# Kernel tuning notes

Measured on AMD Instinct MI355X. Metric: run time of the kernel, lower is better.

Reference implementation:

```python
import jax, jax.numpy as jnp
import numpy as np

HID = 512
J = 64
NEG = -1e9


def _gru_cell(x, h, Wih, Whh, bih, bhh):
    # PyTorch GRUCell: gates stacked as (r, z, n) along first dim of (3H, in)
    gi = Wih @ x + bih          # (3H,)
    gh = Whh @ h + bhh          # (3H,)
    r = jax.nn.sigmoid(gi[:HID] + gh[:HID])
    z = jax.nn.sigmoid(gi[HID:2 * HID] + gh[HID:2 * HID])
    n = jnp.tanh(gi[2 * HID:] + r * gh[2 * HID:])
    return (1.0 - z) * n + z * h


def setup_inputs() -> dict:
    key = jax.random.key(0)
    ks = jax.random.split(key, 8)
    T = 4096
    state_dim = 2 * J  # input is state[t][1:]
    d = {
        "state": jax.random.normal(ks[0], (T, state_dim + 1), dtype=jnp.float32),
        "h_prev": jnp.zeros((2, HID), dtype=jnp.float32),
        "mask": jax.random.randint(ks[1], (J, J), 0, 2, dtype=jnp.int32),
        "Wih0": jax.random.normal(ks[2], (3 * HID, state_dim), dtype=jnp.float32) * 0.05,
        "Whh0": jax.random.normal(ks[3], (3 * HID, HID), dtype=jnp.float32) * 0.04,
        "bih0": jnp.zeros((3 * HID,), dtype=jnp.float32),
        "bhh0": jnp.zeros((3 * HID,), dtype=jnp.float32),
        "Wih1": jax.random.normal(ks[4], (3 * HID, HID), dtype=jnp.float32) * 0.04,
        "Whh1": jax.random.normal(ks[5], (3 * HID, HID), dtype=jnp.float32) * 0.04,
        "bih1": jnp.zeros((3 * HID,), dtype=jnp.float32),
        "bhh1": jnp.zeros((3 * HID,), dtype=jnp.float32),
        "Wfc": jax.random.normal(ks[6], (J * J, HID), dtype=jnp.float32) * 0.06,
        "bfc": jnp.zeros((J * J,), dtype=jnp.float32),
    }
    return d


def reference(state, h_prev, mask, Wih0, Whh0, bih0, bhh0,
              Wih1, Whh1, bih1, bhh1, Wfc, bfc):
    xs = state[:, 1:]  # drop leading element, matches state[t][1:]

    def step(hs, x_t):
        h0 = _gru_cell(x_t, hs[0], Wih0, Whh0, bih0, bhh0)
        h1 = _gru_cell(h0, hs[1], Wih1, Whh1, bih1, bhh1)
        new = jnp.stack([h0, h1])
        return new, h1

    h_next, h_list = jax.lax.scan(step, h_prev, xs)  # h_list: (T, HID)
    logits = jax.nn.relu(h_list @ Wfc.T + bfc)       # (T, J*J)
    logits = logits.reshape(-1, J, J)
    logits = jnp.where(mask == 0, jnp.float32(NEG), logits)
    return logits, h_next
```

## Files before the change

### kernel.cpp

```cpp
#include <hip/hip_runtime.h>
#include <stdint.h>

#define TSTEPS   4096
#define NEG_VAL  -1000000000.0f
#define NWG_SCAN 96
#define G0WG     32
#define RINGN    32

#define GI0_OFF   0
#define H1_OFF    (TSTEPS*1536*4)
#define RING0_OFF (H1_OFF + TSTEPS*512*4)
#define RING1_OFF (RING0_OFF + RINGN*512*8)
#define ARR_OFF   (RING1_OFF + RINGN*512*8)
#define WS_NEED   ((size_t)ARR_OFF + RINGN*64)

static __device__ __forceinline__ unsigned long long ld_a64(const unsigned long long* p){
  return __hip_atomic_load(p, __ATOMIC_RELAXED, __HIP_MEMORY_SCOPE_AGENT);
}
static __device__ __forceinline__ void st_a64(unsigned long long* p, unsigned long long v){
  __hip_atomic_store(p, v, __ATOMIC_RELAXED, __HIP_MEMORY_SCOPE_AGENT);
}
static __device__ __forceinline__ float sigmoidf_(float x){
  return 1.0f / (1.0f + __expf(-x));
}
static __device__ __forceinline__ float tanhf_(float x){
  float ax = fabsf(x);
  float e  = __expf(-2.0f*ax);
  float t  = (1.0f - e) / (1.0f + e);
  return copysignf(t, x);
}

static __device__ __forceinline__ void spin_to_lds(const unsigned long long* ring, int slot,
                                                   unsigned want, int lane, float* dst,
                                                   long* budget){
  const unsigned long long* bp = ring + (size_t)slot*512 + lane;
  unsigned long long v[8];
  for(;;){
    #pragma unroll
    for (int j=0;j<8;++j) v[j] = ld_a64(bp + j*64);
    bool ok = true;
    #pragma unroll
    for (int j=0;j<8;++j) ok = ok && ((unsigned)(v[j]>>32) == want);
    if (ok) break;
    if (--(*budget) < 0) break;
  }
  #pragma unroll
  for (int j=0;j<8;++j) dst[j*64+lane] = __uint_as_float((unsigned)v[j]);
}

__global__ __launch_bounds__(384,1) void gru_scan(
    const float* __restrict__ gi0,
    const float* __restrict__ hprev,
    const float* __restrict__ Whh0,
    const float* __restrict__ Wih1,
    const float* __restrict__ Whh1,
    const float* __restrict__ bhh0,
    const float* __restrict__ bih1,
    const float* __restrict__ bhh1,
    float* __restrict__ H1hist,
    unsigned long long* ring0,
    unsigned long long* ring1,
    unsigned* arr,
    float* __restrict__ hnext)
{
  const int wg   = blockIdx.x;
  const int tid  = threadIdx.x;
  const int wave = tid >> 6;
  const int lane = tid & 63;

  __shared__ float hbuf0[512];
  __shared__ float hbuf1[512];
  __shared__ float sc[64];

  long budget = (1L<<22);

  if (wg < G0WG) {
    const int ibase = wg*16;
    float w[8][8];
    #pragma unroll
    for (int k=0;k<8;++k){
      const int rid = wave*8+k;
      const int g = rid>>4, il = rid&15;
      const float* wp = Whh0 + ((size_t)(g*512 + ibase + il))*512;
      #pragma unroll
      for (int j=0;j<8;++j) w[k][j] = wp[j*64 + lane];
    }
    float hreg=0.f, br=0.f, bz=0.f, bn_=0.f;
    const int mi = ibase + tid;
    if (tid < 16){
      hreg = hprev[mi];
      br  = bhh0[mi]; bz = bhh0[512+mi]; bn_ = bhh0[1024+mi];
    }
    for (int t=0; t<TSTEPS; ++t){
      float gr=0.f, gz=0.f, gn=0.f;
      if (tid < 16){
        const float* gp = gi0 + (size_t)t*1536 + mi;
        gr = gp[0]; gz = gp[512]; gn = gp[1024];
      }
      if (wave == 0){
        if (t == 0){
          #pragma unroll
          for (int j=0;j<8;++j) hbuf0[j*64+lane] = hprev[j*64+lane];
        } else {
          spin_to_lds(ring0, (t-1)&(RINGN-1), (unsigned)t, lane, hbuf0, &budget);
        }
      }
      if (tid==0 && t>=16){
        unsigned* ap = arr + (size_t)((t-16)&(RINGN-1))*16;
        const unsigned expect = (unsigned)NWG_SCAN * (unsigned)(((t-16)>>5)+1);
        while (__hip_atomic_load(ap, __ATOMIC_RELAXED, __HIP_MEMORY_SCOPE_AGENT) < expect){
          if (--budget < 0) break;
        }
      }
      __syncthreads();
      float hj[8];
      #pragma unroll
      for (int j=0;j<8;++j) hj[j] = hbuf0[j*64+lane];
      float acc[8];
      #pragma unroll
      for (int k=0;k<8;++k){
        float a = 0.f;
        #pragma unroll
        for (int j=0;j<8;++j) a = fmaf(w[k][j], hj[j], a);
        #pragma unroll
        for (int off=32; off; off>>=1) a += __shfl_xor(a, off, 64);
        acc[k] = a;
      }
      if (lane == 0){
        #pragma unroll
        for (int k=0;k<8;++k) sc[wave*8+k] = acc[k];
      }
      __syncthreads();
      if (tid < 16){
        const float ghr = sc[tid]    + br;
        const float ghz = sc[16+tid] + bz;
        const float ghn = sc[32+tid] + bn_;
        const float r = sigmoidf_(gr + ghr);
        const float z = sigmoidf_(gz + ghz);
        const float n = tanhf_(gn + r*ghn);
        const float h = (1.f - z)*n + z*hreg;
        hreg = h;
        st_a64(ring0 + (size_t)(t&(RINGN-1))*512 + mi,
               ((unsigned long long)(unsigned)(t+1)<<32) |
               (unsigned long long)__float_as_uint(h));
        if (t == TSTEPS-1) hnext[mi] = h;
      }
      __syncthreads();
      if (tid == 0){
        __hip_atomic_fetch_add(arr + (size_t)(t&(RINGN-1))*16, 1u,
                               __ATOMIC_RELEASE, __HIP_MEMORY_SCOPE_AGENT);
      }
    }
  } else {
    const int wgl = wg - G0WG;
    const int ibase = wgl*8;
    const bool isA = (wave < 3);
    float w[8][8];
    #pragma unroll
    for (int k=0;k<8;++k){
      const int rid = (isA ? wave : (wave-3))*8 + k;
      const int g = rid>>3, il = rid&7;
      const float* W = isA ? Wih1 : Whh1;
      const float* wp = W + ((size_t)(g*512 + ibase + il))*512;
      #pragma unroll
      for (int j=0;j<8;++j) w[k][j] = wp[j*64 + lane];
    }
    float hreg=0.f, bir=0.f,biz=0.f,bin_=0.f, bhr=0.f,bhz=0.f,bhn=0.f;
    const int mi = ibase + tid;
    if (tid < 8){
      hreg = hprev[512+mi];
      bir = bih1[mi]; biz = bih1[512+mi]; bin_ = bih1[1024+mi];
      bhr = bhh1[mi]; bhz = bhh1[512+mi]; bhn  = bhh1[1024+mi];
    }
    for (int s=0; s<TSTEPS; ++s){
      if (wave == 0){
        spin_to_lds(ring0, s&(RINGN-1), (unsigned)(s+1), lane, hbuf0, &budget);
      } else if (wave == 3){
        if (s == 0){
          #pragma unroll
          for (int j=0;j<8;++j) hbuf1[j*64+lane] = hprev[512 + j*64+lane];
        } else {
          spin_to_lds(ring1, (s-1)&(RINGN-1), (unsigned)s, lane, hbuf1, &budget);
        }
      }
      if (tid==0 && s>=16){
        unsigned* ap = arr + (size_t)((s-16)&(RINGN-1))*16;
        const unsigned expect = (unsigned)NWG_SCAN * (unsigned)(((s-16)>>5)+1);
        while (__hip_atomic_load(ap, __ATOMIC_RELAXED, __HIP_MEMORY_SCOPE_AGENT) < expect){
          if (--budget < 0) break;
        }
      }
      __syncthreads();
      const float* hsrc = isA ? hbuf0 : hbuf1;
      float hj[8];
      #pragma unroll
      for (int j=0;j<8;++j) hj[j] = hsrc[j*64+lane];
      float acc[8];
      #pragma unroll
      for (int k=0;k<8;++k){
        float a = 0.f;
        #pragma unroll
        for (int j=0;j<8;++j) a = fmaf(w[k][j], hj[j], a);
        #pragma unroll
        for (int off=32; off; off>>=1) a += __shfl_xor(a, off, 64);
        acc[k] = a;
      }
      if (lane == 0){
        const int base = isA ? (wave*8) : (24 + (wave-3)*8);
        #pragma unroll
        for (int k=0;k<8;++k) sc[base+k] = acc[k];
      }
      __syncthreads();
      if (tid < 8){
        const float gir = sc[tid]    + bir;
        const float giz = sc[8+tid]  + biz;
        const float gin = sc[16+tid] + bin_;
        const float ghr = sc[24+tid] + bhr;
        const float ghz = sc[32+tid] + bhz;
        const float ghn = sc[40+tid] + bhn;
        const float r = sigmoidf_(gir + ghr);
        const float z = sigmoidf_(giz + ghz);
        const float n = tanhf_(gin + r*ghn);
        const float h = (1.f - z)*n + z*hreg;
        hreg = h;
        st_a64(ring1 + (size_t)(s&(RINGN-1))*512 + mi,
               ((unsigned long long)(unsigned)(s+1)<<32) |
               (unsigned long long)__float_as_uint(h));
        H1hist[(size_t)s*512 + mi] = h;
        if (s == TSTEPS-1) hnext[512+mi] = h;
      }
      __syncthreads();
      if (tid == 0){
        __hip_atomic_fetch_add(arr + (size_t)(s&(RINGN-1))*16, 1u,
                               __ATOMIC_RELEASE, __HIP_MEMORY_SCOPE_AGENT);
      }
    }
  }
}

template<int EPI>
__global__ __launch_bounds__(256) void gemm_nt(
    const float* __restrict__ A, int lda,
    const float* __restrict__ B, int ldb,
    float* __restrict__ C, int ldc,
    const float* __restrict__ bias,
    const int* __restrict__ mask,
    int K)
{
  __shared__ __align__(16) float As[32][68];
  __shared__ __align__(16) float Bs[32][68];
  const int bm = blockIdx.y*64, bn = blockIdx.x*64;
  const int tid = threadIdx.x;
  const int tm = tid>>4, tn = tid&15;
  float acc[4][4] = {};
  const int m0 = tid>>2, kk0 = (tid&3)*8;
  for (int k0=0; k0<K; k0+=32){
    #pragma unroll
    for (int j=0;j<8;++j) As[kk0+j][m0] = A[(size_t)(bm+m0)*lda + k0+kk0+j];
    #pragma unroll
    for (int j=0;j<8;++j) Bs[kk0+j][m0] = B[(size_t)(bn+m0)*ldb + k0+kk0+j];
    __syncthreads();
    #pragma unroll
    for (int kk=0;kk<32;++kk){
      const float4 av = *(const float4*)&As[kk][tm*4];
      const float4 bv = *(const float4*)&Bs[kk][tn*4];
      acc[0][0]=fmaf(av.x,bv.x,acc[0][0]); acc[0][1]=fmaf(av.x,bv.y,acc[0][1]);
      acc[0][2]=fmaf(av.x,bv.z,acc[0][2]); acc[0][3]=fmaf(av.x,bv.w,acc[0][3]);
      acc[1][0]=fmaf(av.y,bv.x,acc[1][0]); acc[1][1]=fmaf(av.y,bv.y,acc[1][1]);
      acc[1][2]=fmaf(av.y,bv.z,acc[1][2]); acc[1][3]=fmaf(av.y,bv.w,acc[1][3]);
      acc[2][0]=fmaf(av.z,bv.x,acc[2][0]); acc[2][1]=fmaf(av.z,bv.y,acc[2][1]);
      acc[2][2]=fmaf(av.z,bv.z,acc[2][2]); acc[2][3]=fmaf(av.z,bv.w,acc[2][3]);
      acc[3][0]=fmaf(av.w,bv.x,acc[3][0]); acc[3][1]=fmaf(av.w,bv.y,acc[3][1]);
      acc[3][2]=fmaf(av.w,bv.z,acc[3][2]); acc[3][3]=fmaf(av.w,bv.w,acc[3][3]);
    }
    __syncthreads();
  }
  #pragma unroll
  for (int i=0;i<4;++i){
    #pragma unroll
    for (int j=0;j<4;++j){
      const int mm = bm + tm*4 + i, cc = bn + tn*4 + j;
      float v = acc[i][j] + bias[cc];
      if (EPI){
        v = fmaxf(v, 0.f);
        if (mask[cc] == 0) v = NEG_VAL;
      }
      C[(size_t)mm*ldc + cc] = v;
    }
  }
}

extern "C" void kernel_launch(void* const* d_in, const int* in_sizes, int n_in,
                              void* d_out, int out_size, void* d_ws, size_t ws_size,
                              hipStream_t stream)
{
  const float* state = (const float*)d_in[0];
  const float* hprev = (const float*)d_in[1];
  const int*   mask  = (const int*)d_in[2];
  const float* Wih0  = (const float*)d_in[3];
  const float* Whh0  = (const float*)d_in[4];
  const float* bih0  = (const float*)d_in[5];
  const float* bhh0  = (const float*)d_in[6];
  const float* Wih1  = (const float*)d_in[7];
  const float* Whh1  = (const float*)d_in[8];
  const float* bih1  = (const float*)d_in[9];
  const float* bhh1  = (const float*)d_in[10];
  const float* Wfc   = (const float*)d_in[11];
  const float* bfc   = (const float*)d_in[12];

  if (ws_size < WS_NEED) return;

  float* out = (float*)d_out;
  char*  ws  = (char*)d_ws;
  float* gi0 = (float*)(ws + GI0_OFF);
  float* H1  = (float*)(ws + H1_OFF);
  unsigned long long* ring0 = (unsigned long long*)(ws + RING0_OFF);
  unsigned long long* ring1 = (unsigned long long*)(ws + RING1_OFF);
  unsigned* arr = (unsigned*)(ws + ARR_OFF);

  (void)hipMemsetAsync(ws + RING0_OFF, 0, (size_t)(WS_NEED - RING0_OFF), stream);

  {
    dim3 grid(1536/64, 4096/64);
    gemm_nt<0><<<grid, 256, 0, stream>>>(state+1, 129, Wih0, 128, gi0, 1536,
                                         bih0, nullptr, 128);
  }

  gru_scan<<<NWG_SCAN, 384, 0, stream>>>(gi0, hprev, Whh0, Wih1, Whh1,
                                         bhh0, bih1, bhh1,
                                         H1, ring0, ring1, arr,
                                         out + (size_t)4096*4096);

  {
    dim3 grid(4096/64, 4096/64);
    gemm_nt<1><<<grid, 256, 0, stream>>>(H1, 512, Wfc, 512, out, 4096,
                                         bfc, mask, 512);
  }
}
```

Measured before the change: 12.84 ms.

## Repartition GRU scan into fewer wide workgroups with batched reductions and lighter flow control

The persistent GRU scan now runs on 24 workgroups of 768 threads instead of 96 of 384. Each wave holds 16 weight rows and uses a transpose-style butterfly shuffle reduction (reduce16) in place of a full 64-lane reduction per row. Ring polling is spread over 8 waves, so each lane loads only one word. The per-step atomic arrival counter and its trailing barrier are replaced by per-workgroup progress counters that are published every 4 steps and checked every 8 steps, which should shorten the serial per-step critical path. In exchange each workgroup does more FMA work per step and holds more registers per thread, and the looser ring-overwrite protection depends on the 32-slot ring staying ahead of the lag bound.

Result: slower. 13.94 ms (+8.6%).

```diff
diff --git a/kernel.cpp b/kernel.cpp
--- a/kernel.cpp
+++ b/kernel.cpp
@@ -3,16 +3,17 @@
 
 #define TSTEPS   4096
 #define NEG_VAL  -1000000000.0f
-#define NWG_SCAN 96
-#define G0WG     32
 #define RINGN    32
+#define L0WG     8
+#define L1WG     16
+#define NWG      (L0WG + L1WG)
 
 #define GI0_OFF   0
 #define H1_OFF    (TSTEPS*1536*4)
 #define RING0_OFF (H1_OFF + TSTEPS*512*4)
 #define RING1_OFF (RING0_OFF + RINGN*512*8)
-#define ARR_OFF   (RING1_OFF + RINGN*512*8)
-#define WS_NEED   ((size_t)ARR_OFF + RINGN*64)
+#define PROG_OFF  (RING1_OFF + RINGN*512*8)
+#define WS_NEED   ((size_t)PROG_OFF + NWG*64)
 
 static __device__ __forceinline__ unsigned long long ld_a64(const unsigned long long* p){
   return __hip_atomic_load(p, __ATOMIC_RELAXED, __HIP_MEMORY_SCOPE_AGENT);
@@ -30,25 +31,40 @@
   return copysignf(t, x);
 }
 
-static __device__ __forceinline__ void spin_to_lds(const unsigned long long* ring, int slot,
-                                                   unsigned want, int lane, float* dst,
-                                                   long* budget){
-  const unsigned long long* bp = ring + (size_t)slot*512 + lane;
-  unsigned long long v[8];
-  for(;;){
-    #pragma unroll
-    for (int j=0;j<8;++j) v[j] = ld_a64(bp + j*64);
-    bool ok = true;
-    #pragma unroll
-    for (int j=0;j<8;++j) ok = ok && ((unsigned)(v[j]>>32) == want);
-    if (ok) break;
-    if (--(*budget) < 0) break;
-  }
+static __device__ __forceinline__ float reduce16(const float acc[16], int lane){
+  float s8[8];
   #pragma unroll
-  for (int j=0;j<8;++j) dst[j*64+lane] = __uint_as_float((unsigned)v[j]);
-}
-
-__global__ __launch_bounds__(384,1) void gru_scan(
+  for (int i=0;i<8;++i){
+    float keep = (lane&1) ? acc[8+i] : acc[i];
+    float send = (lane&1) ? acc[i]   : acc[8+i];
+    s8[i] = keep + __shfl_xor(send, 1, 64);
+  }
+  float s4[4];
+  #pragma unroll
+  for (int i=0;i<4;++i){
+    float keep = (lane&2) ? s8[4+i] : s8[i];
+    float send = (lane&2) ? s8[i]   : s8[4+i];
+    s4[i] = keep + __shfl_xor(send, 2, 64);
+  }
+  float s2[2];
+  #pragma unroll
+  for (int i=0;i<2;++i){
+    float keep = (lane&4) ? s4[2+i] : s4[i];
+    float send = (lane&4) ? s4[i]   : s4[2+i];
+    s2[i] = keep + __shfl_xor(send, 4, 64);
+  }
+  float keep = (lane&8) ? s2[1] : s2[0];
+  float send = (lane&8) ? s2[0] : s2[1];
+  float s1 = keep + __shfl_xor(send, 8, 64);
+  s1 += __shfl_xor(s1, 16, 64);
+  s1 += __shfl_xor(s1, 32, 64);
+  return s1;
+}
+static __device__ __forceinline__ int rowmap(int lane){
+  return 8*(lane&1) + 4*((lane>>1)&1) + 2*((lane>>2)&1) + ((lane>>3)&1);
+}
+
+__global__ __launch_bounds__(768,3) void gru_scan(
     const float* __restrict__ gi0,
     const float* __restrict__ hprev,
     const float* __restrict__ Whh0,
@@ -60,7 +76,7 @@
     float* __restrict__ H1hist,
     unsigned long long* ring0,
     unsigned long long* ring1,
-    unsigned* arr,
+    unsigned* prog,
     float* __restrict__ hnext)
 {
   const int wg   = blockIdx.x;
@@ -70,169 +86,179 @@
 
   __shared__ float hbuf0[512];
   __shared__ float hbuf1[512];
-  __shared__ float sc[64];
+  __shared__ float sc[192];
 
   long budget = (1L<<22);
 
-  if (wg < G0WG) {
-    const int ibase = wg*16;
-    float w[8][8];
-    #pragma unroll
-    for (int k=0;k<8;++k){
-      const int rid = wave*8+k;
-      const int g = rid>>4, il = rid&15;
-      const float* wp = Whh0 + ((size_t)(g*512 + ibase + il))*512;
-      #pragma unroll
-      for (int j=0;j<8;++j) w[k][j] = wp[j*64 + lane];
+  if (wg < L0WG) {
+    const int obase = wg*64;
+    float w[16][8];
+    #pragma unroll
+    for (int k=0;k<16;++k){
+      const int r = wave*16 + k;
+      const int g = r >> 6, o = r & 63;
+      const float* wp = Whh0 + ((size_t)(g*512 + obase + o))*512 + lane;
+      #pragma unroll
+      for (int j=0;j<8;++j) w[k][j] = wp[j*64];
     }
     float hreg=0.f, br=0.f, bz=0.f, bn_=0.f;
-    const int mi = ibase + tid;
-    if (tid < 16){
-      hreg = hprev[mi];
-      br  = bhh0[mi]; bz = bhh0[512+mi]; bn_ = bhh0[1024+mi];
+    if (tid < 64){
+      hreg = hprev[obase+tid];
+      br  = bhh0[obase+tid]; bz = bhh0[512+obase+tid]; bn_ = bhh0[1024+obase+tid];
     }
     for (int t=0; t<TSTEPS; ++t){
       float gr=0.f, gz=0.f, gn=0.f;
-      if (tid < 16){
-        const float* gp = gi0 + (size_t)t*1536 + mi;
+      if (tid < 64){
+        const float* gp = gi0 + (size_t)t*1536 + obase + tid;
         gr = gp[0]; gz = gp[512]; gn = gp[1024];
       }
-      if (wave == 0){
+      if (wave < 8){
+        const int word = wave*64 + lane;
         if (t == 0){
-          #pragma unroll
-          for (int j=0;j<8;++j) hbuf0[j*64+lane] = hprev[j*64+lane];
+          hbuf0[word] = hprev[word];
         } else {
-          spin_to_lds(ring0, (t-1)&(RINGN-1), (unsigned)t, lane, hbuf0, &budget);
+          const unsigned long long* p = ring0 + (size_t)((t-1)&(RINGN-1))*512 + word;
+          unsigned long long v;
+          for(;;){ v = ld_a64(p); if ((unsigned)(v>>32) == (unsigned)t) break;
+                   if (--budget < 0) break; }
+          hbuf0[word] = __uint_as_float((unsigned)v);
         }
-      }
-      if (tid==0 && t>=16){
-        unsigned* ap = arr + (size_t)((t-16)&(RINGN-1))*16;
-        const unsigned expect = (unsigned)NWG_SCAN * (unsigned)(((t-16)>>5)+1);
-        while (__hip_atomic_load(ap, __ATOMIC_RELAXED, __HIP_MEMORY_SCOPE_AGENT) < expect){
-          if (--budget < 0) break;
+      } else if (wave == 8 && lane == 0){
+        if ((t & 3) == 0 && t >= 2)
+          __hip_atomic_store(prog + wg*16, (unsigned)(t-2),
+                             __ATOMIC_RELEASE, __HIP_MEMORY_SCOPE_AGENT);
+        if ((t & 7) == 0 && t >= 32){
+          const int need = t - 24;
+          for (int c=0;c<NWG;++c){
+            const unsigned* pp = prog + c*16;
+            while ((int)__hip_atomic_load(pp, __ATOMIC_RELAXED, __HIP_MEMORY_SCOPE_AGENT) < need){
+              if (--budget < 0) break;
+            }
+          }
         }
       }
       __syncthreads();
       float hj[8];
       #pragma unroll
-      for (int j=0;j<8;++j) hj[j] = hbuf0[j*64+lane];
-      float acc[8];
-      #pragma unroll
-      for (int k=0;k<8;++k){
+      for (int j=0;j<8;++j) hj[j] = hbuf0[j*64 + lane];
+      float acc[16];
+      #pragma unroll
+      for (int k=0;k<16;++k){
         float a = 0.f;
         #pragma unroll
         for (int j=0;j<8;++j) a = fmaf(w[k][j], hj[j], a);
-        #pragma unroll
-        for (int off=32; off; off>>=1) a += __shfl_xor(a, off, 64);
         acc[k] = a;
       }
-      if (lane == 0){
-        #pragma unroll
-        for (int k=0;k<8;++k) sc[wave*8+k] = acc[k];
-      }
+      const float s1 = reduce16(acc, lane);
+      if (lane < 16) sc[wave*16 + rowmap(lane)] = s1;
       __syncthreads();
-      if (tid < 16){
-        const float ghr = sc[tid]    + br;
-        const float ghz = sc[16+tid] + bz;
-        const float ghn = sc[32+tid] + bn_;
+      if (tid < 64){
+        const float ghr = sc[tid]     + br;
+        const float ghz = sc[64+tid]  + bz;
+        const float ghn = sc[128+tid] + bn_;
         const float r = sigmoidf_(gr + ghr);
         const float z = sigmoidf_(gz + ghz);
         const float n = tanhf_(gn + r*ghn);
         const float h = (1.f - z)*n + z*hreg;
         hreg = h;
-        st_a64(ring0 + (size_t)(t&(RINGN-1))*512 + mi,
+        st_a64(ring0 + (size_t)(t&(RINGN-1))*512 + obase + tid,
                ((unsigned long long)(unsigned)(t+1)<<32) |
                (unsigned long long)__float_as_uint(h));
-        if (t == TSTEPS-1) hnext[mi] = h;
+        if (t == TSTEPS-1) hnext[obase+tid] = h;
+      }
+    }
+  } else {
+    const int q = wg - L0WG;
+    const int qbase = q*32;
+    float w[16][8];
+    #pragma unroll
+    for (int k=0;k<16;++k){
+      const int rw = wave*16 + k;
+      const bool ih = rw < 96;
+      const int rr = ih ? rw : rw - 96;
+      const int g = rr >> 5, o = rr & 31;
+      const float* W = ih ? Wih1 : Whh1;
+      const float* wp = W + ((size_t)(g*512 + qbase + o))*512 + lane;
+      #pragma unroll
+      for (int j=0;j<8;++j) w[k][j] = wp[j*64];
+    }
+    float hreg=0.f, bir=0.f,biz=0.f,bin_=0.f, bhr=0.f,bhz=0.f,bhn=0.f;
+    if (tid < 32){
+      hreg = hprev[512+qbase+tid];
+      bir = bih1[qbase+tid]; biz = bih1[512+qbase+tid]; bin_ = bih1[1024+qbase+tid];
+      bhr = bhh1[qbase+tid]; bhz = bhh1[512+qbase+tid]; bhn  = bhh1[1024+qbase+tid];
+    }
+    for (int s=0; s<TSTEPS; ++s){
+      if (wave < 8){
+        const int word = wave*64 + lane;
+        const unsigned long long* p = ring0 + (size_t)(s&(RINGN-1))*512 + word;
+        unsigned long long v;
+        for(;;){ v = ld_a64(p); if ((unsigned)(v>>32) == (unsigned)(s+1)) break;
+                 if (--budget < 0) break; }
+        hbuf0[word] = __uint_as_float((unsigned)v);
+      } else {
+        if (wave == 11 && lane == 0){
+          if ((s & 3) == 0 && s >= 1)
+            __hip_atomic_store(prog + wg*16, (unsigned)(s-1),
+                               __ATOMIC_RELEASE, __HIP_MEMORY_SCOPE_AGENT);
+          if ((s & 7) == 0 && s >= 32){
+            const int need = s - 24;
+            for (int c=0;c<NWG;++c){
+              const unsigned* pp = prog + c*16;
+              while ((int)__hip_atomic_load(pp, __ATOMIC_RELAXED, __HIP_MEMORY_SCOPE_AGENT) < need){
+                if (--budget < 0) break;
+              }
+            }
+          }
+        }
+        const int w0 = (wave-8)*128 + lane;
+        if (s == 0){
+          hbuf1[w0]    = hprev[512+w0];
+          hbuf1[w0+64] = hprev[512+w0+64];
+        } else {
+          const unsigned long long* base = ring1 + (size_t)((s-1)&(RINGN-1))*512;
+          unsigned long long v;
+          for(;;){ v = ld_a64(base+w0); if ((unsigned)(v>>32) == (unsigned)s) break;
+                   if (--budget < 0) break; }
+          hbuf1[w0] = __uint_as_float((unsigned)v);
+          for(;;){ v = ld_a64(base+w0+64); if ((unsigned)(v>>32) == (unsigned)s) break;
+                   if (--budget < 0) break; }
+          hbuf1[w0+64] = __uint_as_float((unsigned)v);
+        }
       }
       __syncthreads();
-      if (tid == 0){
-        __hip_atomic_fetch_add(arr + (size_t)(t&(RINGN-1))*16, 1u,
-                               __ATOMIC_RELEASE, __HIP_MEMORY_SCOPE_AGENT);
-      }
-    }
-  } else {
-    const int wgl = wg - G0WG;
-    const int ibase = wgl*8;
-    const bool isA = (wave < 3);
-    float w[8][8];
-    #pragma unroll
-    for (int k=0;k<8;++k){
-      const int rid = (isA ? wave : (wave-3))*8 + k;
-      const int g = rid>>3, il = rid&7;
-      const float* W = isA ? Wih1 : Whh1;
-      const float* wp = W + ((size_t)(g*512 + ibase + il))*512;
-      #pragma unroll
-      for (int j=0;j<8;++j) w[k][j] = wp[j*64 + lane];
-    }
-    float hreg=0.f, bir=0.f,biz=0.f,bin_=0.f, bhr=0.f,bhz=0.f,bhn=0.f;
-    const int mi = ibase + tid;
-    if (tid < 8){
-      hreg = hprev[512+mi];
-      bir = bih1[mi]; biz = bih1[512+mi]; bin_ = bih1[1024+mi];
-      bhr = bhh1[mi]; bhz = bhh1[512+mi]; bhn  = bhh1[1024+mi];
-    }
-    for (int s=0; s<TSTEPS; ++s){
-      if (wave == 0){
-        spin_to_lds(ring0, s&(RINGN-1), (unsigned)(s+1), lane, hbuf0, &budget);
-      } else if (wave == 3){
-        if (s == 0){
-          #pragma unroll
-          for (int j=0;j<8;++j) hbuf1[j*64+lane] = hprev[512 + j*64+lane];
-        } else {
-          spin_to_lds(ring1, (s-1)&(RINGN-1), (unsigned)s, lane, hbuf1, &budget);
-        }
-      }
-      if (tid==0 && s>=16){
-        unsigned* ap = arr + (size_t)((s-16)&(RINGN-1))*16;
-        const unsigned expect = (unsigned)NWG_SCAN * (unsigned)(((s-16)>>5)+1);
-        while (__hip_atomic_load(ap, __ATOMIC_RELAXED, __HIP_MEMORY_SCOPE_AGENT) < expect){
-          if (--budget < 0) break;
-        }
-      }
-      __syncthreads();
-      const float* hsrc = isA ? hbuf0 : hbuf1;
+      const float* hsrc = (wave < 6) ? hbuf0 : hbuf1;
       float hj[8];
       #pragma unroll
-      for (int j=0;j<8;++j) hj[j] = hsrc[j*64+lane];
-      float acc[8];
-      #pragma unroll
-      for (int k=0;k<8;++k){
+      for (int j=0;j<8;++j) hj[j] = hsrc[j*64 + lane];
+      float acc[16];
+      #pragma unroll
+      for (int k=0;k<16;++k){
         float a = 0.f;
         #pragma unroll
         for (int j=0;j<8;++j) a = fmaf(w[k][j], hj[j], a);
-        #pragma unroll
-        for (int off=32; off; off>>=1) a += __shfl_xor(a, off, 64);
         acc[k] = a;
       }
-      if (lane == 0){
-        const int base = isA ? (wave*8) : (24 + (wave-3)*8);
-        #pragma unroll
-        for (int k=0;k<8;++k) sc[base+k] = acc[k];
-      }
+      const float s1 = reduce16(acc, lane);
+      if (lane < 16) sc[wave*16 + rowmap(lane)] = s1;
       __syncthreads();
-      if (tid < 8){
-        const float gir = sc[tid]    + bir;
-        const float giz = sc[8+tid]  + biz;
-        const float gin = sc[16+tid] + bin_;
-        const float ghr = sc[24+tid] + bhr;
-        const float ghz = sc[32+tid] + bhz;
-        const float ghn = sc[40+tid] + bhn;
+      if (tid < 32){
+        const float gir = sc[tid]      + bir;
+        const float giz = sc[32+tid]   + biz;
+        const float gin = sc[64+tid]   + bin_;
+        const float ghr = sc[96+tid]   + bhr;
+        const float ghz = sc[128+tid]  + bhz;
+        const float ghn = sc[160+tid]  + bhn;
         const float r = sigmoidf_(gir + ghr);
         const float z = sigmoidf_(giz + ghz);
         const float n = tanhf_(gin + r*ghn);
         const float h = (1.f - z)*n + z*hreg;
         hreg = h;
-        st_a64(ring1 + (size_t)(s&(RINGN-1))*512 + mi,
+        st_a64(ring1 + (size_t)(s&(RINGN-1))*512 + qbase + tid,
                ((unsigned long long)(unsigned)(s+1)<<32) |
                (unsigned long long)__float_as_uint(h));
-        H1hist[(size_t)s*512 + mi] = h;
-        if (s == TSTEPS-1) hnext[512+mi] = h;
-      }
-      __syncthreads();
-      if (tid == 0){
-        __hip_atomic_fetch_add(arr + (size_t)(s&(RINGN-1))*16, 1u,
-                               __ATOMIC_RELEASE, __HIP_MEMORY_SCOPE_AGENT);
+        H1hist[(size_t)s*512 + qbase + tid] = h;
+        if (s == TSTEPS-1) hnext[512+qbase+tid] = h;
       }
     }
   }
@@ -316,7 +342,7 @@
   float* H1  = (float*)(ws + H1_OFF);
   unsigned long long* ring0 = (unsigned long long*)(ws + RING0_OFF);
   unsigned long long* ring1 = (unsigned long long*)(ws + RING1_OFF);
-  unsigned* arr = (unsigned*)(ws + ARR_OFF);
+  unsigned* prog = (unsigned*)(ws + PROG_OFF);
 
   (void)hipMemsetAsync(ws + RING0_OFF, 0, (size_t)(WS_NEED - RING0_OFF), stream);
 
@@ -326,10 +352,10 @@
                                          bih0, nullptr, 128);
   }
 
-  gru_scan<<<NWG_SCAN, 384, 0, stream>>>(gi0, hprev, Whh0, Wih1, Whh1,
-                                         bhh0, bih1, bhh1,
-                                         H1, ring0, ring1, arr,
-                                         out + (size_t)4096*4096);
+  gru_scan<<<NWG, 768, 0, stream>>>(gi0, hprev, Whh0, Wih1, Whh1,
+                                    bhh0, bih1, bhh1,
+                                    H1, ring0, ring1, prog,
+                                    out + (size_t)4096*4096);
 
   {
     dim3 grid(4096/64, 4096/64);
```
